# Optimization experiments

Measured on AMD Instinct MI355X. Metric: run time of the kernel, lower is better.

## Reference

```python
import jax, jax.numpy as jnp
import numpy as np
import math
from jax.scipy.special import logsumexp

B, S, D, H, L, FF, T, V = 32, 512, 512, 8, 2, 2048, 32, 32000
DH = D // H
LN_EPS = 1e-5
NEG = -1e9


def make_pe(seq_len, d_model):
    pos = np.arange(seq_len, dtype=np.float32)[:, None]
    div = np.exp(np.arange(0, d_model, 2, dtype=np.float32) * (-np.log(10000.0) / d_model))
    pe = np.zeros((seq_len, d_model), np.float32)
    pe[:, 0::2] = np.sin(pos * div)
    pe[:, 1::2] = np.cos(pos * div)
    return jnp.asarray(pe)


def layer_norm(x, scale, bias):
    mu = x.mean(-1, keepdims=True)
    var = ((x - mu) ** 2).mean(-1, keepdims=True)
    return (x - mu) / jnp.sqrt(var + LN_EPS) * scale + bias


def setup_inputs() -> dict:
    key = jax.random.key(0)
    ks = jax.random.split(key, 16)
    w = lambda k, shape, s=0.02: (jax.random.normal(k, shape, dtype=jnp.float32) * s)
    inp = {
        'tokens': jax.random.randint(ks[0], (B, S), 0, V),
        'tags': jax.random.randint(ks[1], (B, S), 0, T),
        'mask': jnp.ones((B, S), dtype=bool),
        'emb': w(ks[2], (V, D)),
        'Wqkv': w(ks[3], (L, 3 * D, D)),
        'bqkv': jnp.zeros((L, 3 * D), jnp.float32),
        'Wo': w(ks[4], (L, D, D)),
        'bo': jnp.zeros((L, D), jnp.float32),
        'ln1_s': jnp.ones((L, D), jnp.float32),
        'ln1_b': jnp.zeros((L, D), jnp.float32),
        'W1': w(ks[5], (L, FF, D)),
        'b1': jnp.zeros((L, FF), jnp.float32),
        'W2': w(ks[6], (L, D, FF)),
        'b2': jnp.zeros((L, D), jnp.float32),
        'ln2_s': jnp.ones((L, D), jnp.float32),
        'ln2_b': jnp.zeros((L, D), jnp.float32),
        'Wtag': w(ks[7], (T, D)),
        'btag': jnp.zeros((T,), jnp.float32),
        'trans': w(ks[8], (T, T), 0.1),
        'start_t': w(ks[9], (T,), 0.1),
        'end_t': w(ks[10], (T,), 0.1),
    }
    return inp


def _forward(tokens, tags, mask, emb, Wqkv, bqkv, Wo, bo, ln1_s, ln1_b, W1, b1, W2, b2,
             ln2_s, ln2_b, Wtag, btag, trans, start_t, end_t):
    # --- embedding + positional encoding ---
    x = emb[tokens] + make_pe(S, D)[None]  # [B,S,D]
    # --- transformer encoder (post-norm, relu, batch_first) ---
    for l in range(L):
        qkv = x @ Wqkv[l].T + bqkv[l]
        q, k, v = jnp.split(qkv, 3, axis=-1)
        q = q.reshape(B, S, H, DH).transpose(0, 2, 1, 3)
        k = k.reshape(B, S, H, DH).transpose(0, 2, 1, 3)
        v = v.reshape(B, S, H, DH).transpose(0, 2, 1, 3)
        scores = jnp.einsum('bhqd,bhkd->bhqk', q, k) / math.sqrt(DH)
        scores = jnp.where(mask[:, None, None, :], scores, NEG)  # key padding mask
        attn = jax.nn.softmax(scores, axis=-1)
        o = jnp.einsum('bhqk,bhkd->bhqd', attn, v).transpose(0, 2, 1, 3).reshape(B, S, D)
        x = layer_norm(x + o @ Wo[l].T + bo[l], ln1_s[l], ln1_b[l])
        h = jax.nn.relu(x @ W1[l].T + b1[l])
        x = layer_norm(x + h @ W2[l].T + b2[l], ln2_s[l], ln2_b[l])
    emissions = x @ Wtag.T + btag  # [B,S,T]

    maskf = mask.astype(emissions.dtype)
    # --- gold path score ---
    emit_sel = jnp.take_along_axis(emissions, tags[..., None], axis=2)[..., 0]  # [B,S]
    trans_sel = trans[tags[:, :-1], tags[:, 1:]]  # [B,S-1]
    score = start_t[tags[:, 0]] + emit_sel[:, 0]
    score = score + jnp.sum((trans_sel + emit_sel[:, 1:]) * maskf[:, 1:], axis=1)
    last_pos = mask.astype(jnp.int32).sum(axis=1) - 1
    last_tags = jnp.take_along_axis(tags, last_pos[:, None], axis=1)[:, 0]
    score = score + end_t[last_tags]

    # --- log partition: forward algorithm as a scan over time ---
    alpha0 = start_t[None] + emissions[:, 0]  # [B,T]

    def step(alpha, inp):
        emit_t, m_t = inp  # [B,T], [B]
        new = logsumexp(alpha[:, :, None] + trans[None] + emit_t[:, None, :], axis=1)
        alpha = jnp.where(m_t[:, None], new, alpha)
        return alpha, None

    alpha, _ = jax.lax.scan(step, alpha0,
                            (emissions[:, 1:].transpose(1, 0, 2), mask[:, 1:].T))
    log_z = logsumexp(alpha + end_t[None], axis=1)
    return (log_z - score).mean()


def reference(tokens, tags, mask, emb, Wqkv, bqkv, Wo, bo, ln1_s, ln1_b, W1, b1, W2, b2,
              ln2_s, ln2_b, Wtag, btag, trans, start_t, end_t):
    return _forward(tokens, tags, mask, emb, Wqkv, bqkv, Wo, bo, ln1_s, ln1_b, W1, b1,
                    W2, b2, ln2_s, ln2_b, Wtag, btag, trans, start_t, end_t)
```

## Files before the change

kernel.cpp:

```cpp
#include <hip/hip_runtime.h>

#define Bz 32
#define Sz 512
#define Dz 512
#define Hz 8
#define Lz 2
#define FFz 2048
#define Tz 32
#define DHz 64

typedef unsigned short u16;
typedef __attribute__((ext_vector_type(8))) short short8;
typedef __attribute__((ext_vector_type(4))) short short4v;
typedef __attribute__((ext_vector_type(4))) float f32x4;

__device__ __forceinline__ float b2f(u16 s) {
    union { unsigned u; float f; } x; x.u = ((unsigned)s) << 16; return x.f;
}
__device__ __forceinline__ u16 f2b(float f) {
    union { float f; unsigned u; } x; x.f = f;
    unsigned r = x.u + 0x7FFFu + ((x.u >> 16) & 1u);
    return (u16)(r >> 16);
}

__device__ __forceinline__ void gload_lds16(const void* g, void* l) {
    __builtin_amdgcn_global_load_lds((const __attribute__((address_space(1))) void*)g,
                                     (__attribute__((address_space(3))) void*)l, 16, 0, 0);
}

template<int BM, int BN, bool OUT_BF16, bool RELU>
__global__ __launch_bounds__(256) void gemm_k(
    const u16* __restrict__ A, int lda, long sAb, long sAh,
    const u16* __restrict__ Bm, int ldb, long sBb, long sBh,
    void* __restrict__ Cm, int ldc, long sCb, long sCh,
    const float* __restrict__ bias,
    const u16* __restrict__ res, int ldres,
    float scale, int K, int nh)
{
    constexpr int WM = BM / 2, WN = BN / 2;
    constexpr int TM = WM / 16, TN = WN / 16;
    __shared__ __align__(16) u16 ldsA[BM * 64];
    __shared__ __align__(16) u16 ldsB[BN * 64];

    const int tid = threadIdx.x, lane = tid & 63, w = tid >> 6;
    const int wm = w >> 1, wn = w & 1;
    const int z = blockIdx.z, zb = z / nh, zh = z % nh;
    A  += (size_t)zb * sAb + (size_t)zh * sAh;
    Bm += (size_t)zb * sBb + (size_t)zh * sBh;
    char* Cc = (char*)Cm + ((size_t)zb * sCb + (size_t)zh * sCh) * (OUT_BF16 ? 2 : 4);

    const int m0 = blockIdx.y * BM, n0 = blockIdx.x * BN;
    f32x4 acc[TM][TN];
#pragma unroll
    for (int mi = 0; mi < TM; ++mi)
#pragma unroll
        for (int ni = 0; ni < TN; ++ni) acc[mi][ni] = (f32x4){0.f, 0.f, 0.f, 0.f};

    const int sr = lane >> 3;
    const int scsw = (((lane & 7) ^ sr) << 3);

    for (int k0 = 0; k0 < K; k0 += 64) {
        const int ra = w * (BM / 4);
#pragma unroll
        for (int t = 0; t < BM / 32; ++t) {
            const u16* g = A + (size_t)(m0 + ra + t * 8 + sr) * lda + k0 + scsw;
            gload_lds16(g, &ldsA[(ra + t * 8) * 64]);
        }
        const int rb = w * (BN / 4);
#pragma unroll
        for (int t = 0; t < BN / 32; ++t) {
            const u16* g = Bm + (size_t)(n0 + rb + t * 8 + sr) * ldb + k0 + scsw;
            gload_lds16(g, &ldsB[(rb + t * 8) * 64]);
        }
        asm volatile("s_waitcnt vmcnt(0)" ::: "memory");
        __syncthreads();
#pragma unroll
        for (int kk = 0; kk < 64; kk += 32) {
            const int kc = (kk >> 3) + (lane >> 4);
            const int sw = ((kc ^ (lane & 7)) << 3);
            short8 af[TM], bf[TN];
#pragma unroll
            for (int mi = 0; mi < TM; ++mi)
                af[mi] = *(const short8*)&ldsA[(wm * WM + mi * 16 + (lane & 15)) * 64 + sw];
#pragma unroll
            for (int ni = 0; ni < TN; ++ni)
                bf[ni] = *(const short8*)&ldsB[(wn * WN + ni * 16 + (lane & 15)) * 64 + sw];
#pragma unroll
            for (int mi = 0; mi < TM; ++mi)
#pragma unroll
                for (int ni = 0; ni < TN; ++ni)
                    acc[mi][ni] = __builtin_amdgcn_mfma_f32_16x16x32_bf16(bf[ni], af[mi], acc[mi][ni], 0, 0, 0);
        }
        __syncthreads();
    }
#pragma unroll
    for (int mi = 0; mi < TM; ++mi) {
        const int m = m0 + wm * WM + mi * 16 + (lane & 15);
#pragma unroll
        for (int ni = 0; ni < TN; ++ni) {
            const int n = n0 + wn * WN + ni * 16 + ((lane >> 4) << 2);
            float v0 = acc[mi][ni][0] * scale, v1 = acc[mi][ni][1] * scale;
            float v2 = acc[mi][ni][2] * scale, v3 = acc[mi][ni][3] * scale;
            if (bias) {
                const float4 b4 = *(const float4*)&bias[n];
                v0 += b4.x; v1 += b4.y; v2 += b4.z; v3 += b4.w;
            }
            if (res) {
                const short4v r4 = *(const short4v*)&res[(size_t)m * ldres + n];
                v0 += b2f((u16)r4[0]); v1 += b2f((u16)r4[1]);
                v2 += b2f((u16)r4[2]); v3 += b2f((u16)r4[3]);
            }
            if (RELU) {
                v0 = fmaxf(v0, 0.f); v1 = fmaxf(v1, 0.f);
                v2 = fmaxf(v2, 0.f); v3 = fmaxf(v3, 0.f);
            }
            if (OUT_BF16) {
                short4v pk;
                pk[0] = (short)f2b(v0); pk[1] = (short)f2b(v1);
                pk[2] = (short)f2b(v2); pk[3] = (short)f2b(v3);
                *(short4v*)&((u16*)Cc)[(size_t)m * ldc + n] = pk;
            } else {
                f32x4 o = (f32x4){v0, v1, v2, v3};
                *(f32x4*)&((float*)Cc)[(size_t)m * ldc + n] = o;
            }
        }
    }
}

__global__ __launch_bounds__(256) void attn_k(const u16* __restrict__ qkv,
                                              const u16* __restrict__ vt,
                                              u16* __restrict__ ao)
{
    __shared__ __align__(16) u16 ldsP[4][32 * 40];
    const int tid = threadIdx.x, lane = tid & 63, w = tid >> 6;
    const int z = blockIdx.x, qt = blockIdx.y;
    const int bb = z >> 3, hh = z & 7;
    const int quad = lane >> 4, c = lane & 15;
    u16* myP = ldsP[w];
    const int q0 = qt * 128 + w * 32;

    const u16* qbase = qkv + (size_t)(bb * Sz + q0) * 1536 + hh * 64;
    short8 qf[2][2];
#pragma unroll
    for (int ni = 0; ni < 2; ++ni)
#pragma unroll
        for (int kk = 0; kk < 2; ++kk)
            qf[ni][kk] = *(const short8*)(qbase + (size_t)(ni * 16 + c) * 1536 + kk * 32 + quad * 8);

    f32x4 oacc[4][2];
    float mst[2] = {-1e30f, -1e30f}, lst[2] = {0.f, 0.f};
#pragma unroll
    for (int i = 0; i < 4; ++i)
#pragma unroll
        for (int j2 = 0; j2 < 2; ++j2) oacc[i][j2] = (f32x4){0.f, 0.f, 0.f, 0.f};

    const u16* kbase = qkv + (size_t)(bb * Sz) * 1536 + 512 + hh * 64;
    const u16* vbase = vt + (size_t)z * (64 * 512);

#pragma unroll 2
    for (int jt = 0; jt < 16; ++jt) {
        const int kv0 = jt * 32;
        short8 kf[2][2];
#pragma unroll
        for (int mi = 0; mi < 2; ++mi)
#pragma unroll
            for (int kk = 0; kk < 2; ++kk)
                kf[mi][kk] = *(const short8*)(kbase + (size_t)(kv0 + mi * 16 + c) * 1536 + kk * 32 + quad * 8);
        f32x4 sacc[2][2];
#pragma unroll
        for (int mi = 0; mi < 2; ++mi)
#pragma unroll
            for (int ni = 0; ni < 2; ++ni) sacc[mi][ni] = (f32x4){0.f, 0.f, 0.f, 0.f};
#pragma unroll
        for (int kk = 0; kk < 2; ++kk)
#pragma unroll
            for (int mi = 0; mi < 2; ++mi)
#pragma unroll
                for (int ni = 0; ni < 2; ++ni)
                    sacc[mi][ni] = __builtin_amdgcn_mfma_f32_16x16x32_bf16(kf[mi][kk], qf[ni][kk], sacc[mi][ni], 0, 0, 0);
        float mnew[2], alpha[2], lad[2];
#pragma unroll
        for (int ni = 0; ni < 2; ++ni) {
            float v = -1e30f;
#pragma unroll
            for (int mi = 0; mi < 2; ++mi)
#pragma unroll
                for (int r = 0; r < 4; ++r) v = fmaxf(v, sacc[mi][ni][r]);
            v *= 0.125f;
            v = fmaxf(v, __shfl_xor(v, 16));
            v = fmaxf(v, __shfl_xor(v, 32));
            mnew[ni] = fmaxf(mst[ni], v);
            alpha[ni] = __expf(mst[ni] - mnew[ni]);
            mst[ni] = mnew[ni];
            lad[ni] = 0.f;
        }
#pragma unroll
        for (int mi = 0; mi < 2; ++mi)
#pragma unroll
            for (int ni = 0; ni < 2; ++ni) {
                float p0 = __expf(sacc[mi][ni][0] * 0.125f - mnew[ni]);
                float p1 = __expf(sacc[mi][ni][1] * 0.125f - mnew[ni]);
                float p2 = __expf(sacc[mi][ni][2] * 0.125f - mnew[ni]);
                float p3 = __expf(sacc[mi][ni][3] * 0.125f - mnew[ni]);
                lad[ni] += (p0 + p1) + (p2 + p3);
                short4v pk;
                pk[0] = (short)f2b(p0); pk[1] = (short)f2b(p1);
                pk[2] = (short)f2b(p2); pk[3] = (short)f2b(p3);
                *(short4v*)&myP[(ni * 16 + c) * 40 + mi * 16 + quad * 4] = pk;
            }
#pragma unroll
        for (int ni = 0; ni < 2; ++ni) {
            float v = lad[ni];
            v += __shfl_xor(v, 16);
            v += __shfl_xor(v, 32);
            lst[ni] = lst[ni] * alpha[ni] + v;
        }
#pragma unroll
        for (int mi2 = 0; mi2 < 4; ++mi2)
#pragma unroll
            for (int ni = 0; ni < 2; ++ni) {
                oacc[mi2][ni][0] *= alpha[ni]; oacc[mi2][ni][1] *= alpha[ni];
                oacc[mi2][ni][2] *= alpha[ni]; oacc[mi2][ni][3] *= alpha[ni];
            }
        short8 vf[4], pf[2];
#pragma unroll
        for (int mi2 = 0; mi2 < 4; ++mi2)
            vf[mi2] = *(const short8*)(vbase + (size_t)(mi2 * 16 + c) * 512 + kv0 + quad * 8);
#pragma unroll
        for (int ni = 0; ni < 2; ++ni)
            pf[ni] = *(const short8*)&myP[(ni * 16 + c) * 40 + quad * 8];
#pragma unroll
        for (int mi2 = 0; mi2 < 4; ++mi2)
#pragma unroll
            for (int ni = 0; ni < 2; ++ni)
                oacc[mi2][ni] = __builtin_amdgcn_mfma_f32_16x16x32_bf16(vf[mi2], pf[ni], oacc[mi2][ni], 0, 0, 0);
    }
    float Linv[2] = {1.f / lst[0], 1.f / lst[1]};
#pragma unroll
    for (int mi2 = 0; mi2 < 4; ++mi2)
#pragma unroll
        for (int ni = 0; ni < 2; ++ni) {
            int q = q0 + ni * 16 + c;
            short4v pk;
#pragma unroll
            for (int r = 0; r < 4; ++r)
                pk[r] = (short)f2b(oacc[mi2][ni][r] * Linv[ni]);
            *(short4v*)&ao[(size_t)(bb * Sz + q) * 512 + hh * 64 + mi2 * 16 + quad * 4] = pk;
        }
}

__global__ __launch_bounds__(256) void prep_k(
    const float* __restrict__ Wqkv, const float* __restrict__ Wo,
    const float* __restrict__ W1, const float* __restrict__ W2,
    const float* __restrict__ wt, const float* __restrict__ bt,
    u16* __restrict__ wqkvb, u16* __restrict__ wob, u16* __restrict__ w1b,
    u16* __restrict__ w2b, u16* __restrict__ wtp, float* __restrict__ btp)
{
    const long n1 = (long)2 * 1536 * 512;
    const long n2 = n1 + (long)2 * 512 * 512;
    const long n3 = n2 + (long)2 * 2048 * 512;
    const long n4 = n3 + (long)2 * 512 * 2048;
    const long n5 = n4 + (long)64 * 512;
    long i = (long)blockIdx.x * 256 + threadIdx.x;
    if (i < n1) wqkvb[i] = f2b(Wqkv[i]);
    else if (i < n2) { long j = i - n1; wob[j] = f2b(Wo[j]); }
    else if (i < n3) { long j = i - n2; w1b[j] = f2b(W1[j]); }
    else if (i < n4) { long j = i - n3; w2b[j] = f2b(W2[j]); }
    else if (i < n5) { long j = i - n4; wtp[j] = ((j >> 9) < Tz) ? f2b(wt[j]) : (u16)0; }
    else if (i < n5 + 64) { long j = i - n5; btp[j] = (j < Tz) ? bt[j] : 0.f; }
}

__global__ __launch_bounds__(256) void embed_k(const int* __restrict__ tokens, const float* __restrict__ emb,
                                               u16* __restrict__ xb) {
    int bs = blockIdx.x * 4 + (threadIdx.x >> 6);
    int lane = threadIdx.x & 63;
    int s = bs & (Sz - 1);
    int tok = tokens[bs];
    const float* er = emb + (size_t)tok * Dz + lane * 8;
    float4 e0 = *(const float4*)er, e1 = *(const float4*)(er + 4);
    float e[8] = {e0.x, e0.y, e0.z, e0.w, e1.x, e1.y, e1.z, e1.w};
    short8 ov;
#pragma unroll
    for (int q = 0; q < 8; ++q) {
        int d = lane * 8 + q;
        int i2 = d & ~1;
        float div = expf(-(float)i2 * (9.210340371976184f / (float)Dz));
        float arg = (float)s * div;
        float pe = (d & 1) ? cosf(arg) : sinf(arg);
        ov[q] = (short)f2b(e[q] + pe);
    }
    *(short8*)&xb[(size_t)bs * Dz + lane * 8] = ov;
}

__global__ __launch_bounds__(256) void ln_k(const float* __restrict__ y, const float* __restrict__ sc,
                                            const float* __restrict__ bi, u16* __restrict__ xb) {
    int row = blockIdx.x * 4 + (threadIdx.x >> 6);
    int lane = threadIdx.x & 63;
    const float* yr = y + (size_t)row * Dz + lane * 8;
    float4 a = *(const float4*)yr, b = *(const float4*)(yr + 4);
    float v[8] = {a.x, a.y, a.z, a.w, b.x, b.y, b.z, b.w};
    float sum = 0.f, sq = 0.f;
#pragma unroll
    for (int q = 0; q < 8; ++q) { sum += v[q]; sq += v[q] * v[q]; }
    for (int o = 32; o; o >>= 1) { sum += __shfl_xor(sum, o); sq += __shfl_xor(sq, o); }
    float mu = sum * (1.f / Dz);
    float var = sq * (1.f / Dz) - mu * mu;
    float rstd = rsqrtf(var + 1e-5f);
    float4 s0 = *(const float4*)&sc[lane * 8], s1 = *(const float4*)&sc[lane * 8 + 4];
    float4 b0 = *(const float4*)&bi[lane * 8], b1 = *(const float4*)&bi[lane * 8 + 4];
    float scv[8] = {s0.x, s0.y, s0.z, s0.w, s1.x, s1.y, s1.z, s1.w};
    float biv[8] = {b0.x, b0.y, b0.z, b0.w, b1.x, b1.y, b1.z, b1.w};
    short8 ov;
#pragma unroll
    for (int q = 0; q < 8; ++q)
        ov[q] = (short)f2b((v[q] - mu) * rstd * scv[q] + biv[q]);
    *(short8*)&xb[(size_t)row * Dz + lane * 8] = ov;
}

__global__ __launch_bounds__(256) void transpose_v_k(const u16* __restrict__ qkv, u16* __restrict__ vt) {
    __shared__ u16 tile[64][72];
    int z = blockIdx.y; int bb = z >> 3, hh = z & 7;
    int s0 = blockIdx.x * 64;
    int t = threadIdx.x;
#pragma unroll
    for (int it = 0; it < 2; ++it) {
        int idx = it * 256 + t;
        int sl = idx >> 3, dv = idx & 7;
        const u16* g = qkv + (size_t)(bb * Sz + s0 + sl) * (3 * Dz) + 2 * Dz + hh * 64 + dv * 8;
        short8 vv = *(const short8*)g;
#pragma unroll
        for (int j = 0; j < 8; ++j) tile[sl][dv * 8 + j] = (u16)vv[j];
    }
    __syncthreads();
#pragma unroll
    for (int it = 0; it < 2; ++it) {
        int idx = it * 256 + t;
        int dh = idx >> 3, sv = idx & 7;
        short8 ov;
#pragma unroll
        for (int j = 0; j < 8; ++j) ov[j] = (short)tile[sv * 8 + j][dh];
        *(short8*)&vt[(size_t)z * DHz * Sz + (size_t)dh * Sz + s0 + sv * 8] = ov;
    }
}

__global__ __launch_bounds__(1024) void crf_span_k(
    const float* __restrict__ emis, const float* __restrict__ trans,
    float* __restrict__ Pout, float* __restrict__ lsout)
{
    __shared__ float E[32 * 32];
    __shared__ float Pb[2][32 * 32];
    __shared__ float wmax[16];
    __shared__ float smax_s, rinv_s, lsum_s;
    const int b = blockIdx.y, s = blockIdx.x;
    const int t0 = 1 + 32 * s;
    const int tend = min(Sz - 1, t0 + 31);
    const int tid = threadIdx.x;
    const int i = tid >> 5, j = tid & 31;
    const int w = tid >> 6;
    const float* em = emis + (size_t)b * Sz * 128;

    E[tid] = __expf(trans[tid]);
    if (tid == 0) { smax_s = 1.f; rinv_s = 1.f; lsum_s = 0.f; }
    __syncthreads();

    float Ecol[32];
#pragma unroll
    for (int k = 0; k < 32; ++k) Ecol[k] = E[k * 32 + j];

    Pb[0][i * 32 + j] = E[i * 32 + j] * __expf(em[(size_t)t0 * 128 + j]);
    __syncthreads();

    int cur = 0;
    float enext = __expf(em[(size_t)(t0 + 1) * 128 + j]);
    for (int t = t0 + 1; t <= tend; ++t) {
        float e = enext;
        if (t < tend) enext = __expf(em[(size_t)(t + 1) * 128 + j]);
        const float* Pr = &Pb[cur][i * 32];
        float v = 0.f;
#pragma unroll
        for (int k = 0; k < 32; ++k) v += Pr[k] * Ecol[k];
        v *= e * rinv_s;
        Pb[1 - cur][i * 32 + j] = v;
        float m = v;
        for (int o = 32; o; o >>= 1) m = fmaxf(m, __shfl_xor(m, o));
        if ((tid & 63) == 0) wmax[w] = m;
        __syncthreads();
        if (tid == 0) {
            float bm = wmax[0];
#pragma unroll
            for (int q = 1; q < 16; ++q) bm = fmaxf(bm, wmax[q]);
            lsum_s += __logf(smax_s);
            smax_s = bm;
            rinv_s = 1.f / bm;
        }
        __syncthreads();
        cur ^= 1;
    }
    Pout[(((size_t)b * 16 + s) * 32 + i) * 32 + j] = Pb[cur][i * 32 + j];
    if (tid == 0) lsout[b * 16 + s] = lsum_s;
}

__global__ __launch_bounds__(64) void crf2_k(
    const float* __restrict__ emis, const int* __restrict__ tags,
    const float* __restrict__ trans, const float* __restrict__ start_t,
    const float* __restrict__ end_t, const float* __restrict__ Pspan,
    const float* __restrict__ lsspan, float* __restrict__ diff)
{
    const int b = blockIdx.x, lane = threadIdx.x;
    const int* tg = tags + b * Sz;
    const float* em = emis + (size_t)b * Sz * 128;
    float partial = 0.f;
    for (int t = 1 + lane; t < Sz; t += 64) {
        int tp = tg[t - 1], tc = tg[t];
        partial += trans[tp * Tz + tc] + em[(size_t)t * 128 + tc];
    }
    for (int o = 32; o; o >>= 1) partial += __shfl_xor(partial, o);
    float score = partial + start_t[tg[0]] + em[tg[0]] + end_t[tg[Sz - 1]];

    const int j = lane & 31, hb = lane & 32;
    float a0 = start_t[j] + em[j];
    float m0 = a0;
    for (int o = 16; o; o >>= 1) m0 = fmaxf(m0, __shfl_xor(m0, o));
    float a = __expf(a0 - m0);
    float ls = m0;

    const float* Pb_ = Pspan + (size_t)b * 16 * 1024;
    float Pc[32];
#pragma unroll
    for (int k = 0; k < 32; ++k) Pc[k] = Pb_[k * 32 + j];
    for (int s = 0; s < 16; ++s) {
        float Pn[32];
        if (s < 15) {
#pragma unroll
            for (int k = 0; k < 32; ++k) Pn[k] = Pb_[(s + 1) * 1024 + k * 32 + j];
        }
        float an = 0.f;
#pragma unroll
        for (int k = 0; k < 32; ++k) an += __shfl(a, hb + k) * Pc[k];
        float am = an;
        for (int o = 16; o; o >>= 1) am = fmaxf(am, __shfl_xor(am, o));
        a = an / am;
        ls += __logf(am) + lsspan[b * 16 + s];
#pragma unroll
        for (int k = 0; k < 32; ++k) Pc[k] = Pn[k];
    }
    float wv = a * __expf(end_t[j]);
    for (int o = 16; o; o >>= 1) wv += __shfl_xor(wv, o);
    float logz = ls + __logf(wv);
    if (lane == 0) diff[b] = logz - score;
}

__global__ __launch_bounds__(64) void reduce_k(const float* __restrict__ diff, float* __restrict__ out) {
    int lane = threadIdx.x;
    float v = (lane < Bz) ? diff[lane] : 0.f;
    for (int o = 32; o; o >>= 1) v += __shfl_xor(v, o);
    if (lane == 0) out[0] = v / (float)Bz;
}

__global__ void sentinel_k(float* out, float v) {
    if (threadIdx.x == 0) out[0] = v;
}

extern "C" void kernel_launch(void* const* d_in, const int* in_sizes, int n_in,
                              void* d_out, int out_size, void* d_ws, size_t ws_size,
                              hipStream_t stream) {
    const int*   tokens = (const int*)d_in[0];
    const int*   tags   = (const int*)d_in[1];
    const float* emb    = (const float*)d_in[3];
    const float* Wqkv   = (const float*)d_in[4];
    const float* bqkv   = (const float*)d_in[5];
    const float* Wo     = (const float*)d_in[6];
    const float* bo     = (const float*)d_in[7];
    const float* ln1s   = (const float*)d_in[8];
    const float* ln1b   = (const float*)d_in[9];
    const float* W1     = (const float*)d_in[10];
    const float* b1     = (const float*)d_in[11];
    const float* W2     = (const float*)d_in[12];
    const float* b2     = (const float*)d_in[13];
    const float* ln2s   = (const float*)d_in[14];
    const float* ln2b   = (const float*)d_in[15];
    const float* Wtag   = (const float*)d_in[16];
    const float* btag   = (const float*)d_in[17];
    const float* trans  = (const float*)d_in[18];
    const float* start_t= (const float*)d_in[19];
    const float* end_t  = (const float*)d_in[20];

    char* base = (char*)d_ws;
    size_t off = 0;
    auto alloc = [&](size_t bytes) -> void* {
        void* p = base + off;
        off += (bytes + 255) & ~(size_t)255;
        return p;
    };
    u16*   xb    = (u16*)  alloc((size_t)16384 * 512 * 2);
    u16*   qkv   = (u16*)  alloc((size_t)16384 * 1536 * 2);
    u16*   vt    = (u16*)  alloc((size_t)256 * 64 * 512 * 2);
    u16*   ao    = (u16*)  alloc((size_t)16384 * 512 * 2);
    u16*   wqkvb = (u16*)  alloc((size_t)2 * 1536 * 512 * 2);
    u16*   wob   = (u16*)  alloc((size_t)2 * 512 * 512 * 2);
    u16*   w1b   = (u16*)  alloc((size_t)2 * 2048 * 512 * 2);
    u16*   w2b   = (u16*)  alloc((size_t)2 * 512 * 2048 * 2);
    u16*   wtagb = (u16*)  alloc((size_t)64 * 512 * 2);
    float* btagp = (float*)alloc(256);
    float* diff  = (float*)alloc(256);
    u16*   scratch=(u16*)  alloc((size_t)16384 * 2048 * 2);
    float* y     = (float*)qkv;
    float* emis  = (float*)ao;
    float* Pspan = (float*)scratch;
    float* lsspan= (float*)(scratch + 1048576);

    if (off > ws_size) {
        sentinel_k<<<1, 64, 0, stream>>>((float*)d_out, (float)ws_size);
        return;
    }

    {
        long total = (long)2 * 1536 * 512 + (long)2 * 512 * 512 + (long)2 * 2048 * 512
                   + (long)2 * 512 * 2048 + (long)64 * 512 + 64;
        prep_k<<<(int)((total + 255) / 256), 256, 0, stream>>>(
            Wqkv, Wo, W1, W2, Wtag, btag, wqkvb, wob, w1b, w2b, wtagb, btagp);
    }
    embed_k<<<4096, 256, 0, stream>>>(tokens, emb, xb);

    for (int l = 0; l < Lz; ++l) {
        gemm_k<128, 128, true, false><<<dim3(12, 128, 1), 256, 0, stream>>>(
            xb, 512, 0, 0, wqkvb + (size_t)l * 1536 * 512, 512, 0, 0,
            qkv, 1536, 0, 0, bqkv + l * 1536, nullptr, 0, 1.f, 512, 1);
        transpose_v_k<<<dim3(8, 256), 256, 0, stream>>>(qkv, vt);
        attn_k<<<dim3(256, 4), 256, 0, stream>>>(qkv, vt, ao);
        gemm_k<128, 128, false, false><<<dim3(4, 128, 1), 256, 0, stream>>>(
            ao, 512, 0, 0, wob + (size_t)l * 512 * 512, 512, 0, 0,
            y, 512, 0, 0, bo + l * 512, xb, 512, 1.f, 512, 1);
        ln_k<<<4096, 256, 0, stream>>>(y, ln1s + l * 512, ln1b + l * 512, xb);
        gemm_k<128, 128, true, true><<<dim3(16, 128, 1), 256, 0, stream>>>(
            xb, 512, 0, 0, w1b + (size_t)l * 2048 * 512, 512, 0, 0,
            scratch, 2048, 0, 0, b1 + l * 2048, nullptr, 0, 1.f, 512, 1);
        gemm_k<128, 128, false, false><<<dim3(4, 128, 1), 256, 0, stream>>>(
            scratch, 2048, 0, 0, w2b + (size_t)l * 512 * 2048, 2048, 0, 0,
            y, 512, 0, 0, b2 + l * 512, xb, 512, 1.f, 2048, 1);
        ln_k<<<4096, 256, 0, stream>>>(y, ln2s + l * 512, ln2b + l * 512, xb);
    }
    gemm_k<128, 64, false, false><<<dim3(1, 128, 1), 256, 0, stream>>>(
        xb, 512, 0, 0, wtagb, 512, 0, 0,
        emis, 128, 0, 0, btagp, nullptr, 0, 1.f, 512, 1);
    crf_span_k<<<dim3(16, Bz), 1024, 0, stream>>>(emis, trans, Pspan, lsspan);
    crf2_k<<<Bz, 64, 0, stream>>>(emis, tags, trans, start_t, end_t, Pspan, lsspan, diff);
    reduce_k<<<1, 64, 0, stream>>>(diff, (float*)d_out);
}
```

Before: 803.0 us.

## Compute CRF span matrix products with bf16 MFMA in a single wavefront

```diff
diff --git a/kernel.cpp b/kernel.cpp
--- a/kernel.cpp
+++ b/kernel.cpp
@@ -343,61 +343,101 @@
     }
 }
 
-__global__ __launch_bounds__(1024) void crf_span_k(
+__global__ __launch_bounds__(64) void crf_span_k(
     const float* __restrict__ emis, const float* __restrict__ trans,
     float* __restrict__ Pout, float* __restrict__ lsout)
 {
-    __shared__ float E[32 * 32];
-    __shared__ float Pb[2][32 * 32];
-    __shared__ float wmax[16];
-    __shared__ float smax_s, rinv_s, lsum_s;
+    __shared__ __align__(16) u16 Pm[32 * 40];
+    const int lane = threadIdx.x;
     const int b = blockIdx.y, s = blockIdx.x;
     const int t0 = 1 + 32 * s;
     const int tend = min(Sz - 1, t0 + 31);
-    const int tid = threadIdx.x;
-    const int i = tid >> 5, j = tid & 31;
-    const int w = tid >> 6;
+    const int quad = lane >> 4, c = lane & 15;
     const float* em = emis + (size_t)b * Sz * 128;
 
-    E[tid] = __expf(trans[tid]);
-    if (tid == 0) { smax_s = 1.f; rinv_s = 1.f; lsum_s = 0.f; }
+    float ebf[2][8];
+#pragma unroll
+    for (int cj = 0; cj < 2; ++cj)
+#pragma unroll
+        for (int jj = 0; jj < 8; ++jj)
+            ebf[cj][jj] = __expf(trans[(quad * 8 + jj) * 32 + cj * 16 + c]);
+
+    {
+        int i = lane >> 1;
+        int jb = (lane & 1) * 16;
+#pragma unroll
+        for (int q = 0; q < 16; ++q) {
+            int j = jb + q;
+            float v = __expf(trans[i * 32 + j]) * __expf(em[(size_t)t0 * 128 + j]);
+            Pm[i * 40 + j] = f2b(v);
+        }
+    }
     __syncthreads();
 
-    float Ecol[32];
-#pragma unroll
-    for (int k = 0; k < 32; ++k) Ecol[k] = E[k * 32 + j];
-
-    Pb[0][i * 32 + j] = E[i * 32 + j] * __expf(em[(size_t)t0 * 128 + j]);
-    __syncthreads();
-
-    int cur = 0;
-    float enext = __expf(em[(size_t)(t0 + 1) * 128 + j]);
+    float smax = 1.f, lsum = 0.f;
+    float e0 = em[(size_t)(t0 + 1) * 128 + c];
+    float e1 = em[(size_t)(t0 + 1) * 128 + 16 + c];
     for (int t = t0 + 1; t <= tend; ++t) {
-        float e = enext;
-        if (t < tend) enext = __expf(em[(size_t)(t + 1) * 128 + j]);
-        const float* Pr = &Pb[cur][i * 32];
-        float v = 0.f;
-#pragma unroll
-        for (int k = 0; k < 32; ++k) v += Pr[k] * Ecol[k];
-        v *= e * rinv_s;
-        Pb[1 - cur][i * 32 + j] = v;
-        float m = v;
-        for (int o = 32; o; o >>= 1) m = fmaxf(m, __shfl_xor(m, o));
-        if ((tid & 63) == 0) wmax[w] = m;
+        float rinv = 1.f / smax;
+        float s0 = __expf(e0) * rinv, s1 = __expf(e1) * rinv;
+        if (t < tend) {
+            e0 = em[(size_t)(t + 1) * 128 + c];
+            e1 = em[(size_t)(t + 1) * 128 + 16 + c];
+        }
+        short8 mb[2];
+#pragma unroll
+        for (int jj = 0; jj < 8; ++jj) {
+            mb[0][jj] = (short)f2b(ebf[0][jj] * s0);
+            mb[1][jj] = (short)f2b(ebf[1][jj] * s1);
+        }
+        short8 pa[2];
+        pa[0] = *(const short8*)&Pm[c * 40 + quad * 8];
+        pa[1] = *(const short8*)&Pm[(16 + c) * 40 + quad * 8];
+        f32x4 C[2][2];
+#pragma unroll
+        for (int ri = 0; ri < 2; ++ri)
+#pragma unroll
+            for (int cj = 0; cj < 2; ++cj)
+                C[ri][cj] = __builtin_amdgcn_mfma_f32_16x16x32_bf16(
+                    pa[ri], mb[cj], (f32x4){0.f, 0.f, 0.f, 0.f}, 0, 0, 0);
+        float bm = -1e30f;
+#pragma unroll
+        for (int ri = 0; ri < 2; ++ri)
+#pragma unroll
+            for (int cj = 0; cj < 2; ++cj)
+#pragma unroll
+                for (int r = 0; r < 4; ++r) bm = fmaxf(bm, C[ri][cj][r]);
+        for (int o = 32; o; o >>= 1) bm = fmaxf(bm, __shfl_xor(bm, o));
+        lsum += __logf(smax);
+        smax = bm;
         __syncthreads();
-        if (tid == 0) {
-            float bm = wmax[0];
-#pragma unroll
-            for (int q = 1; q < 16; ++q) bm = fmaxf(bm, wmax[q]);
-            lsum_s += __logf(smax_s);
-            smax_s = bm;
-            rinv_s = 1.f / bm;
-        }
-        __syncthreads();
-        cur ^= 1;
-    }
-    Pout[(((size_t)b * 16 + s) * 32 + i) * 32 + j] = Pb[cur][i * 32 + j];
-    if (tid == 0) lsout[b * 16 + s] = lsum_s;
+        if (t < tend) {
+#pragma unroll
+            for (int ri = 0; ri < 2; ++ri)
+#pragma unroll
+                for (int cj = 0; cj < 2; ++cj)
+#pragma unroll
+                    for (int r = 0; r < 4; ++r) {
+                        int i = ri * 16 + quad * 4 + r;
+                        int j = cj * 16 + c;
+                        Pm[i * 40 + j] = f2b(C[ri][cj][r]);
+                    }
+            __syncthreads();
+        } else {
+            float* Po = Pout + (((size_t)b * 16 + s) * 1024);
+#pragma unroll
+            for (int ri = 0; ri < 2; ++ri)
+#pragma unroll
+                for (int cj = 0; cj < 2; ++cj)
+#pragma unroll
+                    for (int r = 0; r < 4; ++r) {
+                        int i = ri * 16 + quad * 4 + r;
+                        int j = cj * 16 + c;
+                        Po[i * 32 + j] = C[ri][cj][r];
+                    }
+        }
+    }
+    if (lane == 0) lsout[b * 16 + s] = lsum;
 }
 
 __global__ __launch_bounds__(64) void crf2_k(
@@ -543,7 +583,7 @@
     gemm_k<128, 64, false, false><<<dim3(1, 128, 1), 256, 0, stream>>>(
         xb, 512, 0, 0, wtagb, 512, 0, 0,
         emis, 128, 0, 0, btagp, nullptr, 0, 1.f, 512, 1);
-    crf_span_k<<<dim3(16, Bz), 1024, 0, stream>>>(emis, trans, Pspan, lsspan);
+    crf_span_k<<<dim3(16, Bz), 64, 0, stream>>>(emis, trans, Pspan, lsspan);
     crf2_k<<<Bz, 64, 0, stream>>>(emis, tags, trans, start_t, end_t, Pspan, lsspan, diff);
     reduce_k<<<1, 64, 0, stream>>>(diff, (float*)d_out);
 }
```

Measured after the change: 745.7 us. 1.08x faster.
